# Optimization experiments

Measured on AMD Instinct MI355X. Metric: run time of the kernel, lower is better.

## Reference

```python
import jax, jax.numpy as jnp
import numpy as np

B, T, C = 32, 1024, 8
K, LH, SIGMA = 10, 32, 1.0
TCN_CH = [32, 64, 128]
KS = 3
TCN_OUT, FUS_H, REG_H, HOR = 64, 256, 128, 10


def _causal_conv(x, w, b, dilation):
    # x: (B, Cin, T), w: (Cout, Cin, K) ; left-pad == torch symmetric pad + Chomp1d
    pad = (w.shape[-1] - 1) * dilation
    y = jax.lax.conv_general_dilated(x, w, (1,), [(pad, 0)], rhs_dilation=(dilation,),
                                     dimension_numbers=('NCH', 'OIH', 'NCH'))
    return y + b[None, :, None]


def _temporal_block(x, c1w, c1b, c2w, c2b, dw, db, dilation):
    out = jax.nn.relu(_causal_conv(x, c1w, c1b, dilation))
    out = jax.nn.relu(_causal_conv(out, c2w, c2b, dilation))
    res = _causal_conv(x, dw, db, 1)  # 1x1 downsample (in_ch != out_ch at every block here)
    return jax.nn.relu(out + res)


def _laplace(x, pw, pb, ow, ob):
    h = x @ pw + pb  # (B,T,LH)
    sq = jnp.sum(h * h, axis=-1)  # (B,T)
    d2 = sq[:, :, None] + sq[:, None, :] - 2.0 * jnp.einsum('bth,bsh->bts', h, h)
    d2 = jnp.maximum(d2, 0.0)
    d2 = d2 + 1e18 * jnp.eye(h.shape[1], dtype=h.dtype)[None]  # exclude self, like diagonal fill 1e9
    _, idx = jax.lax.top_k(-jax.lax.stop_gradient(d2), K)  # (B,T,K) smallest distances
    neigh = jax.vmap(lambda hb, ib: hb[ib])(h, idx)  # (B,T,K,LH) gather
    diff = neigh - h[:, :, None, :]
    # w = exp(-||diff||^2 / (2 sigma^2 + 1e-8)); computed from squared norm directly (same math)
    w = jnp.exp(-jnp.sum(diff * diff, axis=-1) / (2.0 * SIGMA ** 2 + 1e-8))  # (B,T,K)
    w = w / (jnp.sum(w, axis=-1, keepdims=True) + 1e-8)
    smooth = jnp.einsum('btk,btkh->bth', w, neigh)
    lap = h - smooth
    return jnp.tanh(lap) @ ow + ob  # (B,T,LH)


def _forward(x, pw, pb, ow, ob,
             b0_c1w, b0_c1b, b0_c2w, b0_c2b, b0_dw, b0_db,
             b1_c1w, b1_c1b, b1_c2w, b1_c2b, b1_dw, b1_db,
             b2_c1w, b2_c1b, b2_c2w, b2_c2b, b2_dw, b2_db,
             head_w, head_b, f1w, f1b, f2w, f2b, r1w, r1b, r2w, r2b):
    lap_feat = _laplace(x, pw, pb, ow, ob)
    lap_pool = jnp.mean(lap_feat, axis=1)  # (B,LH)
    y = jnp.transpose(x, (0, 2, 1))  # (B,C,T)
    y = _temporal_block(y, b0_c1w, b0_c1b, b0_c2w, b0_c2b, b0_dw, b0_db, 1)
    y = _temporal_block(y, b1_c1w, b1_c1b, b1_c2w, b1_c2b, b1_dw, b1_db, 2)
    y = _temporal_block(y, b2_c1w, b2_c1b, b2_c2w, b2_c2b, b2_dw, b2_db, 4)
    tcn_feat = y[:, :, -1] @ head_w + head_b  # (B,TCN_OUT)
    fused = jnp.concatenate([lap_pool, tcn_feat], axis=-1)  # (B, LH+TCN_OUT)
    fused = jax.nn.relu(fused @ f1w + f1b)
    fused = jax.nn.relu(fused @ f2w + f2b)
    h = jax.nn.relu(fused @ r1w + r1b)
    return h @ r2w + r2b  # (B, HOR)


def setup_inputs() -> dict:
    key = jax.random.key(0)
    ks = iter(jax.random.split(key, 64))

    def p(shape, scale=0.05):
        return jax.random.normal(next(ks), shape, dtype=jnp.float32) * scale

    inp = {'x': jax.random.normal(next(ks), (B, T, C), dtype=jnp.float32)}
    inp['pw'] = p((C, LH)); inp['pb'] = p((LH,))
    inp['ow'] = p((LH, LH)); inp['ob'] = p((LH,))
    chans = [C] + TCN_CH
    for i in range(3):
        ci, co = chans[i], chans[i + 1]
        inp['b%d_c1w' % i] = p((co, ci, KS)); inp['b%d_c1b' % i] = p((co,))
        inp['b%d_c2w' % i] = p((co, co, KS)); inp['b%d_c2b' % i] = p((co,))
        inp['b%d_dw' % i] = p((co, ci, 1)); inp['b%d_db' % i] = p((co,))
    inp['head_w'] = p((TCN_CH[-1], TCN_OUT)); inp['head_b'] = p((TCN_OUT,))
    inp['f1w'] = p((LH + TCN_OUT, FUS_H)); inp['f1b'] = p((FUS_H,))
    inp['f2w'] = p((FUS_H, FUS_H)); inp['f2b'] = p((FUS_H,))
    inp['r1w'] = p((FUS_H, REG_H)); inp['r1b'] = p((REG_H,))
    inp['r2w'] = p((REG_H, HOR)); inp['r2b'] = p((HOR,))
    return inp


def reference(x, pw, pb, ow, ob,
              b0_c1w, b0_c1b, b0_c2w, b0_c2b, b0_dw, b0_db,
              b1_c1w, b1_c1b, b1_c2w, b1_c2b, b1_dw, b1_db,
              b2_c1w, b2_c1b, b2_c2w, b2_c2b, b2_dw, b2_db,
              head_w, head_b, f1w, f1b, f2w, f2b, r1w, r1b, r2w, r2b):
    return _forward(x, pw, pb, ow, ob,
                    b0_c1w, b0_c1b, b0_c2w, b0_c2b, b0_dw, b0_db,
                    b1_c1w, b1_c1b, b1_c2w, b1_c2b, b1_dw, b1_db,
                    b2_c1w, b2_c1b, b2_c2w, b2_c2b, b2_dw, b2_db,
                    head_w, head_b, f1w, f1b, f2w, f2b, r1w, r1b, r2w, r2b)
```

## Files before the change

kernel.cpp:

```cpp
#include <hip/hip_runtime.h>
#include <hip/hip_bf16.h>

#define B_  32
#define T_  1024
#define C_  8
#define K_  10
#define LH_ 32

#define WS_H    0
#define WS_SQ   1048576
#define WS_ACC  (WS_SQ + 32768)
#define WS_WT   (WS_ACC + 1024)
#define WS_Y    (WS_WT + 106496)

#define WT_C1_0 0
#define WT_C2_0 768
#define WT_DW0  3840
#define WT_C1_1 4096
#define WT_C2_1 10240
#define WT_DW1  22528
#define WT_C1_2 24576
#define WT_C2_2 49152
#define WT_DW2  98304
#define WT_TOTAL 106496

#define PROJ_BLOCKS ((B_ * T_ * LH_) / 256)
#define WT_BLOCKS   ((WT_TOTAL + 255) / 256)

struct WSegs { const float* src[9]; int k3[9]; int colog2[9]; int off[10]; };

__global__ __launch_bounds__(256) void k_project(
    const float* __restrict__ x,
    const float* __restrict__ pw,
    const float* __restrict__ pb,
    float* __restrict__ h, float* __restrict__ sq, float* __restrict__ acc,
    WSegs S, float* __restrict__ wT)
{
    if (blockIdx.x >= PROJ_BLOCKS) {
        int gid = (blockIdx.x - PROJ_BLOCKS) * 256 + threadIdx.x;
        if (gid < WT_TOTAL) {
#pragma unroll
            for (int s = 0; s < 9; ++s) {
                if (gid >= S.off[s] && gid < S.off[s + 1]) {
                    int local = gid - S.off[s];
                    int k = local >> S.colog2[s];
                    int o = local & ((1 << S.colog2[s]) - 1);
                    wT[gid] = S.src[s][o * S.k3[s] + k];
                }
            }
        }
        return;
    }

    int gid = blockIdx.x * 256 + threadIdx.x;
    if (gid < B_ * LH_) acc[gid] = 0.f;
    int row = gid >> 5;
    int i   = gid & 31;
    const float* xr = x + (size_t)row * C_;
    float4 x0 = *(const float4*)xr;
    float4 x1 = *(const float4*)(xr + 4);
    float hv = pb[i];
    hv = fmaf(x0.x, pw[0 * LH_ + i], hv);
    hv = fmaf(x0.y, pw[1 * LH_ + i], hv);
    hv = fmaf(x0.z, pw[2 * LH_ + i], hv);
    hv = fmaf(x0.w, pw[3 * LH_ + i], hv);
    hv = fmaf(x1.x, pw[4 * LH_ + i], hv);
    hv = fmaf(x1.y, pw[5 * LH_ + i], hv);
    hv = fmaf(x1.z, pw[6 * LH_ + i], hv);
    hv = fmaf(x1.w, pw[7 * LH_ + i], hv);
    h[(size_t)row * LH_ + i] = hv;
    float e = hv * hv;
#pragma unroll
    for (int off = 1; off < 32; off <<= 1) e += __shfl_xor(e, off, 64);
    if (i == 0) sq[row] = e;
}

__device__ __forceinline__ unsigned wave_min_u32(unsigned v)
{
#define DPP_MIN(ctrl) \
    v = min(v, (unsigned)__builtin_amdgcn_update_dpp((int)v, (int)v, ctrl, 0xF, 0xF, false))
    DPP_MIN(0x111);
    DPP_MIN(0x112);
    DPP_MIN(0x114);
    DPP_MIN(0x118);
    DPP_MIN(0x142);
    DPP_MIN(0x143);
#undef DPP_MIN
    return (unsigned)__builtin_amdgcn_readlane((int)v, 63);
}

struct TcnW {
    const float *x;
    const float *c1b0, *c2b0, *db0;
    const float *c1b1, *c2b1, *db1;
    const float *c1b2, *c2b2, *db2;
};

__device__ void tcn_block(int b, const TcnW& W, const float* __restrict__ wT,
                          float* sm, float* y, int tid)
{
    float* xw = sm;
    float* a0 = sm + 232;
    float* o0 = sm + 1096;
    float* a1 = sm + 1896;
    float* o1 = sm + 3240;
    float* a2 = sm + 4328;

    if (tid < 232) xw[tid] = W.x[(size_t)b * (T_ * C_) + 995 * C_ + tid];
    __syncthreads();

#pragma unroll 1
    for (int e = tid; e < 27 * 32; e += 256) {
        int r = e >> 5, o = e & 31;
        const float* wr = wT + WT_C1_0;
        float s = W.c1b0[o];
#pragma unroll
        for (int i = 0; i < 8; ++i)
#pragma unroll
            for (int j = 0; j < 3; ++j)
                s = fmaf(wr[(i * 3 + j) * 32 + o], xw[(r + j) * 8 + i], s);
        a0[e] = fmaxf(s, 0.f);
    }
    __syncthreads();

#pragma unroll 1
    for (int e = tid; e < 25 * 32; e += 256) {
        int r = e >> 5, o = e & 31;
        const float* wr = wT + WT_C2_0;
        float s = W.c2b0[o];
#pragma unroll 4
        for (int i = 0; i < 32; ++i)
#pragma unroll
            for (int j = 0; j < 3; ++j)
                s = fmaf(wr[(i * 3 + j) * 32 + o], a0[(r + j) * 32 + i], s);
        s = fmaxf(s, 0.f);
        const float* dr = wT + WT_DW0;
        float rs = W.db0[o];
#pragma unroll
        for (int i = 0; i < 8; ++i)
            rs = fmaf(dr[i * 32 + o], xw[(4 + r) * 8 + i], rs);
        o0[e] = fmaxf(s + rs, 0.f);
    }
    __syncthreads();

#pragma unroll 1
    for (int e = tid; e < 21 * 64; e += 256) {
        int r = e >> 6, o = e & 63;
        const float* wr = wT + WT_C1_1;
        float s = W.c1b1[o];
#pragma unroll 4
        for (int i = 0; i < 32; ++i)
#pragma unroll
            for (int j = 0; j < 3; ++j)
                s = fmaf(wr[(i * 3 + j) * 64 + o], o0[(r + 2 * j) * 32 + i], s);
        a1[e] = fmaxf(s, 0.f);
    }
    __syncthreads();

#pragma unroll 1
    for (int e = tid; e < 17 * 64; e += 256) {
        int r = e >> 6, o = e & 63;
        const float* wr = wT + WT_C2_1;
        float s = W.c2b1[o];
#pragma unroll 4
        for (int i = 0; i < 64; ++i)
#pragma unroll
            for (int j = 0; j < 3; ++j)
                s = fmaf(wr[(i * 3 + j) * 64 + o], a1[(r + 2 * j) * 64 + i], s);
        s = fmaxf(s, 0.f);
        const float* dr = wT + WT_DW1;
        float rs = W.db1[o];
#pragma unroll 4
        for (int i = 0; i < 32; ++i)
            rs = fmaf(dr[i * 64 + o], o0[(8 + r) * 32 + i], rs);
        o1[e] = fmaxf(s + rs, 0.f);
    }
    __syncthreads();

#pragma unroll 1
    for (int e = tid; e < 9 * 128; e += 256) {
        int r = e >> 7, o = e & 127;
        const float* wr = wT + WT_C1_2;
        float s = W.c1b2[o];
#pragma unroll 4
        for (int i = 0; i < 64; ++i)
#pragma unroll
            for (int j = 0; j < 3; ++j)
                s = fmaf(wr[(i * 3 + j) * 128 + o], o1[(r + 4 * j) * 64 + i], s);
        a2[e] = fmaxf(s, 0.f);
    }
    __syncthreads();

    if (tid < 128) {
        int o = tid;
        const float* wr = wT + WT_C2_2;
        float s = W.c2b2[o];
#pragma unroll 4
        for (int i = 0; i < 128; ++i)
#pragma unroll
            for (int j = 0; j < 3; ++j)
                s = fmaf(wr[(i * 3 + j) * 128 + o], a2[(4 * j) * 128 + i], s);
        s = fmaxf(s, 0.f);
        const float* dr = wT + WT_DW2;
        float rs = W.db2[o];
#pragma unroll 4
        for (int i = 0; i < 64; ++i)
            rs = fmaf(dr[i * 128 + o], o1[16 * 64 + i], rs);
        y[(size_t)b * 128 + o] = fmaxf(s + rs, 0.f);
    }
}

#define STILE 128
#define SPAD  36
#define TCN_BLOCKS 32
#define NTILE (T_ / STILE)

__global__ __launch_bounds__(256, 2) void k_laplace(
    const float* __restrict__ h, const float* __restrict__ sq,
    float* __restrict__ acc, TcnW tw, const float* __restrict__ wT,
    float* __restrict__ y)
{
    __shared__ float tile[2][STILE * SPAD];
    __shared__ float wacc[4 * 32];
    __shared__ float qbuf[8 * 32];

    if (blockIdx.x < TCN_BLOCKS) {
        tcn_block(blockIdx.x, tw, wT, &tile[0][0], y, threadIdx.x);
        return;
    }
    const int bid = blockIdx.x - TCN_BLOCKS;

    const int tid = threadIdx.x;
    const int wv  = tid >> 6;
    const int ln  = tid & 63;
    const int b   = bid >> 7;
    const int t0  = (bid & 127) * 8;
    const int tA  = t0 + wv * 2;
    const int tB  = tA + 1;

    const float* hb  = h  + (size_t)b * T_ * LH_;
    const float* sqb = sq + b * T_;

    if (ln < 32) {
        qbuf[(wv * 2 + 0) * 32 + ln] = hb[tA * LH_ + ln];
        qbuf[(wv * 2 + 1) * 32 + ln] = hb[tB * LH_ + ln];
    }
    float qA[32], qB[32];
#pragma unroll
    for (int i4 = 0; i4 < 8; ++i4) {
        float4 a4 = *(const float4*)(hb + (size_t)tA * LH_ + i4 * 4);
        float4 b4 = *(const float4*)(hb + (size_t)tB * LH_ + i4 * 4);
        qA[i4 * 4 + 0] = a4.x; qA[i4 * 4 + 1] = a4.y;
        qA[i4 * 4 + 2] = a4.z; qA[i4 * 4 + 3] = a4.w;
        qB[i4 * 4 + 0] = b4.x; qB[i4 * 4 + 1] = b4.y;
        qB[i4 * 4 + 2] = b4.z; qB[i4 * 4 + 3] = b4.w;
    }
    const float sqA = sqb[tA], sqB = sqb[tB];

    const int st_r  = tid >> 3, st_c4 = tid & 7;
    auto stage = [&](int buf, int s_base) {
#pragma unroll
        for (int u = 0; u < 4; ++u) {
            int r = st_r + u * 32;
            float4 val = *(const float4*)(hb + (size_t)(s_base + r) * LH_ + st_c4 * 4);
            *(float4*)&tile[buf][r * SPAD + st_c4 * 4] = val;
        }
    };

    unsigned kA[16], kB[16];

    stage(0, 0);
    __syncthreads();

    for (int tl = 0; tl < NTILE; ++tl) {
        const int s_base = tl * STILE;
        const int cur = tl & 1;
        if (tl + 1 < NTILE) stage(cur ^ 1, s_base + STILE);
#pragma unroll
        for (int sub = 0; sub < 2; ++sub) {
            const int sr = sub * 64 + ln;
            const int s  = s_base + sr;
            const float* hs = &tile[cur][sr * SPAD];
            float dA = 0.f, dB = 0.f;
#pragma unroll
            for (int q4 = 0; q4 < 8; ++q4) {
                float4 hv4 = *(const float4*)(hs + q4 * 4);
                dA = fmaf(hv4.x, qA[q4 * 4 + 0], dA); dB = fmaf(hv4.x, qB[q4 * 4 + 0], dB);
                dA = fmaf(hv4.y, qA[q4 * 4 + 1], dA); dB = fmaf(hv4.y, qB[q4 * 4 + 1], dB);
                dA = fmaf(hv4.z, qA[q4 * 4 + 2], dA); dB = fmaf(hv4.z, qB[q4 * 4 + 2], dB);
                dA = fmaf(hv4.w, qA[q4 * 4 + 3], dA); dB = fmaf(hv4.w, qB[q4 * 4 + 3], dB);
            }
            const float sqs = sqb[s];
            float d2A = fmaxf(sqA + sqs - 2.f * dA, 0.f);
            float d2B = fmaxf(sqB + sqs - 2.f * dB, 0.f);
            unsigned keyA = (__float_as_uint(d2A) & 0xFFFFFC00u) | (unsigned)s;
            unsigned keyB = (__float_as_uint(d2B) & 0xFFFFFC00u) | (unsigned)s;
            if (s == tA) keyA = 0xFFFFFC00u | (unsigned)s;
            if (s == tB) keyB = 0xFFFFFC00u | (unsigned)s;
            kA[tl * 2 + sub] = keyA;
            kB[tl * 2 + sub] = keyB;
        }
        if (tl + 1 < NTILE) __syncthreads();
    }

    float racc = 0.f;

    auto process = [&](unsigned (&ku)[16], int qslot) {
#pragma unroll
        for (int k = 2; k <= 16; k <<= 1) {
#pragma unroll
            for (int j = k >> 1; j > 0; j >>= 1) {
#pragma unroll
                for (int i = 0; i < 16; ++i) {
                    int l = i ^ j;
                    if (l > i) {
                        unsigned a = ku[i], bb = ku[l];
                        unsigned mn = min(a, bb), mx = max(a, bb);
                        bool up = ((i & k) == 0);
                        ku[i] = up ? mn : mx;
                        ku[l] = up ? mx : mn;
                    }
                }
            }
        }
        int   sk[K_];
        float wk[K_];
#pragma unroll
        for (int r = 0; r < K_; ++r) {
            unsigned mu = wave_min_u32(ku[0]);
            int s_win = (int)(mu & 1023u);
            sk[r] = s_win;
            wk[r] = __expf(-0.5f * __uint_as_float(mu & 0xFFFFFC00u));
            const bool winlane = ((s_win & 63) == ln);
#pragma unroll
            for (int i = 0; i < 10; ++i)
                ku[i] = winlane ? ku[i + 1] : ku[i];
            ku[10] = winlane ? 0xFFFFFFFFu : ku[10];
        }
        const int i = ln & 31;
        const float qi = qbuf[qslot * 32 + i];
        float W = 0.f, sm = 0.f;
#pragma unroll
        for (int k = 0; k < K_; ++k) {
            W += wk[k];
            sm = fmaf(wk[k], hb[(size_t)sk[k] * LH_ + i], sm);
        }
        sm *= __builtin_amdgcn_rcpf(W + 1e-8f);
        float z  = qi - sm;
        float ex = __expf(2.f * z);
        racc += 1.f - 2.f * __builtin_amdgcn_rcpf(ex + 1.f);
    };

    process(kA, wv * 2 + 0);
    process(kB, wv * 2 + 1);

    if (ln < 32) wacc[wv * 32 + ln] = racc;
    __syncthreads();
    if (tid < 32) {
        float tot = wacc[tid] + wacc[32 + tid] + wacc[64 + tid] + wacc[96 + tid];
        atomicAdd(&acc[b * LH_ + tid], tot);
    }
}

struct HeadW {
    const float *ow, *ob, *head_w, *head_b;
    const float *f1w, *f1b, *f2w, *f2b, *r1w, *r1b, *r2w, *r2b;
};

__global__ __launch_bounds__(256) void k_head(
    const float* __restrict__ y, const float* __restrict__ acc,
    HeadW hw, float* __restrict__ out)
{
    const int b = blockIdx.x, tid = threadIdx.x;
    __shared__ float yv[128], v96[96], h1[256], h2[256], h3[128];

    if (tid < 128) yv[tid] = y[b * 128 + tid];
    else if (tid < 160) {
        int j = tid - 128;
        float s = hw.ob[j];
        for (int i = 0; i < 32; ++i)
            s = fmaf(acc[b * 32 + i] * (1.f / 1024.f), hw.ow[i * 32 + j], s);
        v96[j] = s;
    }
    __syncthreads();
    if (tid < 64) {
        float s = hw.head_b[tid];
        for (int i = 0; i < 128; ++i)
            s = fmaf(yv[i], hw.head_w[i * 64 + tid], s);
        v96[32 + tid] = s;
    }
    __syncthreads();
    {
        float s = hw.f1b[tid];
        for (int i = 0; i < 96; ++i)
            s = fmaf(v96[i], hw.f1w[i * 256 + tid], s);
        h1[tid] = fmaxf(s, 0.f);
    }
    __syncthreads();
    {
        float s = hw.f2b[tid];
        for (int i = 0; i < 256; ++i)
            s = fmaf(h1[i], hw.f2w[i * 256 + tid], s);
        h2[tid] = fmaxf(s, 0.f);
    }
    __syncthreads();
    if (tid < 128) {
        float s = hw.r1b[tid];
        for (int i = 0; i < 256; ++i)
            s = fmaf(h2[i], hw.r1w[i * 128 + tid], s);
        h3[tid] = fmaxf(s, 0.f);
    }
    __syncthreads();
    if (tid < 10) {
        float s = hw.r2b[tid];
        for (int i = 0; i < 128; ++i)
            s = fmaf(h3[i], hw.r2w[i * 10 + tid], s);
        out[b * 10 + tid] = s;
    }
}

extern "C" void kernel_launch(void* const* d_in, const int* in_sizes, int n_in,
                              void* d_out, int out_size, void* d_ws, size_t ws_size,
                              hipStream_t stream)
{
    const float* x  = (const float*)d_in[0];
    const float* pw = (const float*)d_in[1];
    const float* pb = (const float*)d_in[2];

    const float* c1w0 = (const float*)d_in[5];  const float* c1b0 = (const float*)d_in[6];
    const float* c2w0 = (const float*)d_in[7];  const float* c2b0 = (const float*)d_in[8];
    const float* dw0  = (const float*)d_in[9];  const float* db0  = (const float*)d_in[10];
    const float* c1w1 = (const float*)d_in[11]; const float* c1b1 = (const float*)d_in[12];
    const float* c2w1 = (const float*)d_in[13]; const float* c2b1 = (const float*)d_in[14];
    const float* dw1  = (const float*)d_in[15]; const float* db1  = (const float*)d_in[16];
    const float* c1w2 = (const float*)d_in[17]; const float* c1b2 = (const float*)d_in[18];
    const float* c2w2 = (const float*)d_in[19]; const float* c2b2 = (const float*)d_in[20];
    const float* dw2  = (const float*)d_in[21]; const float* db2  = (const float*)d_in[22];

    TcnW tw;
    tw.x    = x;
    tw.c1b0 = c1b0; tw.c2b0 = c2b0; tw.db0 = db0;
    tw.c1b1 = c1b1; tw.c2b1 = c2b1; tw.db1 = db1;
    tw.c1b2 = c1b2; tw.c2b2 = c2b2; tw.db2 = db2;

    HeadW hw = { (const float*)d_in[3],  (const float*)d_in[4],
                 (const float*)d_in[23], (const float*)d_in[24],
                 (const float*)d_in[25], (const float*)d_in[26],
                 (const float*)d_in[27], (const float*)d_in[28],
                 (const float*)d_in[29], (const float*)d_in[30],
                 (const float*)d_in[31], (const float*)d_in[32] };

    float* W   = (float*)d_ws;
    float* h   = W + WS_H;
    float* sq  = W + WS_SQ;
    float* acc = W + WS_ACC;
    float* wT  = W + WS_WT;
    float* y   = W + WS_Y;

    WSegs S;
    const float* srcs[9] = {c1w0, c2w0, dw0, c1w1, c2w1, dw1, c1w2, c2w2, dw2};
    const int k3s[9]   = {24, 96, 8, 96, 192, 32, 192, 384, 64};
    const int col2[9]  = {5, 5, 5, 6, 6, 6, 7, 7, 7};
    const int offs[10] = {WT_C1_0, WT_C2_0, WT_DW0, WT_C1_1, WT_C2_1, WT_DW1,
                          WT_C1_2, WT_C2_2, WT_DW2, WT_TOTAL};
    for (int i = 0; i < 9; ++i) { S.src[i] = srcs[i]; S.k3[i] = k3s[i]; S.colog2[i] = col2[i]; }
    for (int i = 0; i < 10; ++i) S.off[i] = offs[i];

    k_project<<<PROJ_BLOCKS + WT_BLOCKS, 256, 0, stream>>>(x, pw, pb, h, sq, acc, S, wT);
    k_laplace<<<(B_ * T_) / 8 + TCN_BLOCKS, 256, 0, stream>>>(h, sq, acc, tw, wT, y);
    k_head<<<B_, 256, 0, stream>>>(y, acc, hw, (float*)d_out);
}
```

Baseline: 229.5 us.

## Fuse head MLP into laplace kernel via last-block-arrives counter

Removes the separate k_head launch. Each laplace or TCN block increments a per-batch atomic counter after writing its results. The last of the 129 arrivals for a batch then runs the head MLP inline, reusing the block's shared-memory tile. This saves one kernel launch and its inter-kernel gap, at the cost of extra threadfences and atomics in every block, and a serialized tail MLP run by one block per batch.

Measured after the change: 477.8 us. 2.08x slower.

```diff
diff --git a/kernel.cpp b/kernel.cpp
--- a/kernel.cpp
+++ b/kernel.cpp
@@ -12,6 +12,7 @@
 #define WS_ACC  (WS_SQ + 32768)
 #define WS_WT   (WS_ACC + 1024)
 #define WS_Y    (WS_WT + 106496)
+#define WS_CNT  (WS_Y + 4096)
 
 #define WT_C1_0 0
 #define WT_C2_0 768
@@ -34,6 +35,7 @@
     const float* __restrict__ pw,
     const float* __restrict__ pb,
     float* __restrict__ h, float* __restrict__ sq, float* __restrict__ acc,
+    unsigned* __restrict__ cnt,
     WSegs S, float* __restrict__ wT)
 {
     if (blockIdx.x >= PROJ_BLOCKS) {
@@ -54,6 +56,7 @@
 
     int gid = blockIdx.x * 256 + threadIdx.x;
     if (gid < B_ * LH_) acc[gid] = 0.f;
+    if (gid < B_) cnt[gid] = 0u;
     int row = gid >> 5;
     int i   = gid & 31;
     const float* xr = x + (size_t)row * C_;
@@ -89,6 +92,72 @@
     return (unsigned)__builtin_amdgcn_readlane((int)v, 63);
 }
 
+struct HeadW {
+    const float *ow, *ob, *head_w, *head_b;
+    const float *f1w, *f1b, *f2w, *f2b, *r1w, *r1b, *r2w, *r2b;
+};
+
+__device__ void head_body(int b, const float* __restrict__ y,
+                          const float* __restrict__ acc, const HeadW& hw,
+                          float* __restrict__ out, float* sm, int tid)
+{
+    float* yv  = sm;
+    float* v96 = sm + 128;
+    float* h1  = sm + 224;
+    float* h2  = sm + 480;
+    float* h3  = sm + 736;
+
+    if (tid < 128) yv[tid] = y[b * 128 + tid];
+    else if (tid < 160) {
+        int j = tid - 128;
+        float s = hw.ob[j];
+#pragma unroll 1
+        for (int i = 0; i < 32; ++i)
+            s = fmaf(acc[b * 32 + i] * (1.f / 1024.f), hw.ow[i * 32 + j], s);
+        v96[j] = s;
+    }
+    __syncthreads();
+    if (tid < 64) {
+        float s = hw.head_b[tid];
+#pragma unroll 1
+        for (int i = 0; i < 128; ++i)
+            s = fmaf(yv[i], hw.head_w[i * 64 + tid], s);
+        v96[32 + tid] = s;
+    }
+    __syncthreads();
+    {
+        float s = hw.f1b[tid];
+#pragma unroll 1
+        for (int i = 0; i < 96; ++i)
+            s = fmaf(v96[i], hw.f1w[i * 256 + tid], s);
+        h1[tid] = fmaxf(s, 0.f);
+    }
+    __syncthreads();
+    {
+        float s = hw.f2b[tid];
+#pragma unroll 1
+        for (int i = 0; i < 256; ++i)
+            s = fmaf(h1[i], hw.f2w[i * 256 + tid], s);
+        h2[tid] = fmaxf(s, 0.f);
+    }
+    __syncthreads();
+    if (tid < 128) {
+        float s = hw.r1b[tid];
+#pragma unroll 1
+        for (int i = 0; i < 256; ++i)
+            s = fmaf(h2[i], hw.r1w[i * 128 + tid], s);
+        h3[tid] = fmaxf(s, 0.f);
+    }
+    __syncthreads();
+    if (tid < 10) {
+        float s = hw.r2b[tid];
+#pragma unroll 1
+        for (int i = 0; i < 128; ++i)
+            s = fmaf(h3[i], hw.r2w[i * 10 + tid], s);
+        out[b * 10 + tid] = s;
+    }
+}
+
 struct TcnW {
     const float *x;
     const float *c1b0, *c2b0, *db0;
@@ -214,18 +283,33 @@
 #define SPAD  36
 #define TCN_BLOCKS 32
 #define NTILE (T_ / STILE)
+#define ARRIVALS_PER_BATCH 129
 
 __global__ __launch_bounds__(256, 2) void k_laplace(
     const float* __restrict__ h, const float* __restrict__ sq,
-    float* __restrict__ acc, TcnW tw, const float* __restrict__ wT,
-    float* __restrict__ y)
+    float* __restrict__ acc, unsigned* __restrict__ cnt,
+    TcnW tw, const float* __restrict__ wT,
+    float* __restrict__ y, HeadW hw, float* __restrict__ out)
 {
     __shared__ float tile[2][STILE * SPAD];
     __shared__ float wacc[4 * 32];
     __shared__ float qbuf[8 * 32];
+    __shared__ int lastflag;
 
     if (blockIdx.x < TCN_BLOCKS) {
-        tcn_block(blockIdx.x, tw, wT, &tile[0][0], y, threadIdx.x);
+        const int bb = blockIdx.x;
+        tcn_block(bb, tw, wT, &tile[0][0], y, threadIdx.x);
+        __syncthreads();
+        if (threadIdx.x == 0) {
+            __threadfence();
+            unsigned c = atomicAdd(&cnt[bb], 1u);
+            lastflag = (c == ARRIVALS_PER_BATCH - 1);
+        }
+        __syncthreads();
+        if (lastflag) {
+            __threadfence();
+            head_body(bb, y, acc, hw, out, &tile[0][0], threadIdx.x);
+        }
         return;
     }
     const int bid = blockIdx.x - TCN_BLOCKS;
@@ -360,62 +444,17 @@
         float tot = wacc[tid] + wacc[32 + tid] + wacc[64 + tid] + wacc[96 + tid];
         atomicAdd(&acc[b * LH_ + tid], tot);
     }
-}
-
-struct HeadW {
-    const float *ow, *ob, *head_w, *head_b;
-    const float *f1w, *f1b, *f2w, *f2b, *r1w, *r1b, *r2w, *r2b;
-};
-
-__global__ __launch_bounds__(256) void k_head(
-    const float* __restrict__ y, const float* __restrict__ acc,
-    HeadW hw, float* __restrict__ out)
-{
-    const int b = blockIdx.x, tid = threadIdx.x;
-    __shared__ float yv[128], v96[96], h1[256], h2[256], h3[128];
-
-    if (tid < 128) yv[tid] = y[b * 128 + tid];
-    else if (tid < 160) {
-        int j = tid - 128;
-        float s = hw.ob[j];
-        for (int i = 0; i < 32; ++i)
-            s = fmaf(acc[b * 32 + i] * (1.f / 1024.f), hw.ow[i * 32 + j], s);
-        v96[j] = s;
-    }
-    __syncthreads();
-    if (tid < 64) {
-        float s = hw.head_b[tid];
-        for (int i = 0; i < 128; ++i)
-            s = fmaf(yv[i], hw.head_w[i * 64 + tid], s);
-        v96[32 + tid] = s;
-    }
-    __syncthreads();
-    {
-        float s = hw.f1b[tid];
-        for (int i = 0; i < 96; ++i)
-            s = fmaf(v96[i], hw.f1w[i * 256 + tid], s);
-        h1[tid] = fmaxf(s, 0.f);
-    }
-    __syncthreads();
-    {
-        float s = hw.f2b[tid];
-        for (int i = 0; i < 256; ++i)
-            s = fmaf(h1[i], hw.f2w[i * 256 + tid], s);
-        h2[tid] = fmaxf(s, 0.f);
-    }
-    __syncthreads();
-    if (tid < 128) {
-        float s = hw.r1b[tid];
-        for (int i = 0; i < 256; ++i)
-            s = fmaf(h2[i], hw.r1w[i * 128 + tid], s);
-        h3[tid] = fmaxf(s, 0.f);
-    }
-    __syncthreads();
-    if (tid < 10) {
-        float s = hw.r2b[tid];
-        for (int i = 0; i < 128; ++i)
-            s = fmaf(h3[i], hw.r2w[i * 10 + tid], s);
-        out[b * 10 + tid] = s;
+
+    __syncthreads();
+    if (tid == 0) {
+        __threadfence();
+        unsigned c = atomicAdd(&cnt[b], 1u);
+        lastflag = (c == ARRIVALS_PER_BATCH - 1);
+    }
+    __syncthreads();
+    if (lastflag) {
+        __threadfence();
+        head_body(b, y, acc, hw, out, &tile[0][0], tid);
     }
 }
 
@@ -450,12 +489,13 @@
                  (const float*)d_in[29], (const float*)d_in[30],
                  (const float*)d_in[31], (const float*)d_in[32] };
 
-    float* W   = (float*)d_ws;
-    float* h   = W + WS_H;
-    float* sq  = W + WS_SQ;
-    float* acc = W + WS_ACC;
-    float* wT  = W + WS_WT;
-    float* y   = W + WS_Y;
+    float* W    = (float*)d_ws;
+    float* h    = W + WS_H;
+    float* sq   = W + WS_SQ;
+    float* acc  = W + WS_ACC;
+    float* wT   = W + WS_WT;
+    float* y    = W + WS_Y;
+    unsigned* cnt = (unsigned*)(W + WS_CNT);
 
     WSegs S;
     const float* srcs[9] = {c1w0, c2w0, dw0, c1w1, c2w1, dw1, c1w2, c2w2, dw2};
@@ -466,7 +506,7 @@
     for (int i = 0; i < 9; ++i) { S.src[i] = srcs[i]; S.k3[i] = k3s[i]; S.colog2[i] = col2[i]; }
     for (int i = 0; i < 10; ++i) S.off[i] = offs[i];
 
-    k_project<<<PROJ_BLOCKS + WT_BLOCKS, 256, 0, stream>>>(x, pw, pb, h, sq, acc, S, wT);
-    k_laplace<<<(B_ * T_) / 8 + TCN_BLOCKS, 256, 0, stream>>>(h, sq, acc, tw, wT, y);
-    k_head<<<B_, 256, 0, stream>>>(y, acc, hw, (float*)d_out);
+    k_project<<<PROJ_BLOCKS + WT_BLOCKS, 256, 0, stream>>>(x, pw, pb, h, sq, acc, cnt, S, wT);
+    k_laplace<<<(B_ * T_) / 8 + TCN_BLOCKS, 256, 0, stream>>>(
+        h, sq, acc, cnt, tw, wT, y, hw, (float*)d_out);
 }
```
